# Kernel optimization log

Measured on AMD Instinct MI355X. Metric: run time of the kernel, lower is better.

The kernel has to match this reference:

```python
import jax, jax.numpy as jnp
import numpy as np

# Mamba config (HF defaults for hidden_size=256)
VOCAB = 4096
H = 256          # hidden_size
I = 512          # intermediate_size = 2*H
N = 16           # state_size
R = 16           # time_step_rank = ceil(H/16)
K = 4            # conv_kernel
NUM_LAYERS = 4
B, L = 4, 1024
EPS = 1e-5


def _rmsnorm(x, w):
    return x * jax.lax.rsqrt(jnp.mean(x * x, axis=-1, keepdims=True) + EPS) * w


def setup_inputs() -> dict:
    key = jax.random.key(0)
    ks = jax.random.split(key, 20)
    s = 0.02
    Lyr = NUM_LAYERS
    inp = {
        'input_ids': jax.random.randint(ks[0], (B, L), 0, VOCAB),
        'lengths': jax.random.randint(ks[1], (B,), 1, L + 1),
        'embed': jax.random.normal(ks[2], (VOCAB, H)) * s,
        'norm_w': jnp.ones((Lyr, H)),
        'in_proj_w': jax.random.normal(ks[3], (Lyr, 2 * I, H)) * s,
        'conv_w': jax.random.normal(ks[4], (Lyr, I, K)) * s,
        'conv_b': jnp.zeros((Lyr, I)),
        'x_proj_w': jax.random.normal(ks[5], (Lyr, R + 2 * N, I)) * s,
        'dt_proj_w': jax.random.normal(ks[6], (Lyr, I, R)) * s,
        'dt_proj_b': jax.random.normal(ks[7], (Lyr, I)) * 0.5 - 4.0,
        'A_log': jnp.log(jnp.broadcast_to(jnp.arange(1, N + 1, dtype=jnp.float32), (Lyr, I, N))),
        'D': jnp.ones((Lyr, I)),
        'out_proj_w': jax.random.normal(ks[8], (Lyr, H, I)) * s,
        'final_norm_w': jnp.ones((H,)),
        'head_w1': jax.random.normal(ks[9], (H // 4, H)) * s,
        'head_b1': jnp.zeros((H // 4,)),
        'head_w2': jax.random.normal(ks[10], (1, H // 4)) * s,
        'head_b2': jnp.zeros((1,)),
    }
    return inp


def _mixer(x, in_proj_w, conv_w, conv_b, x_proj_w, dt_proj_w, dt_proj_b, A_log, D_, out_proj_w):
    b, l, _ = x.shape
    proj = x @ in_proj_w.T                      # (b,l,2I)
    xs, gate = proj[..., :I], proj[..., I:]
    # depthwise causal conv1d (kernel K, left pad K-1)
    xp = jnp.pad(xs, ((0, 0), (K - 1, 0), (0, 0)))
    conv = sum(xp[:, k:k + l, :] * conv_w[:, k] for k in range(K))
    xs = jax.nn.silu(conv + conv_b)             # (b,l,I)
    ssm = xs @ x_proj_w.T                       # (b,l,R+2N)
    dt_r, Bmat, Cmat = ssm[..., :R], ssm[..., R:R + N], ssm[..., R + N:]
    dt = jax.nn.softplus(dt_r @ dt_proj_w.T + dt_proj_b)   # (b,l,I)
    A = -jnp.exp(A_log)                         # (I,N)
    dA = jnp.exp(dt[..., None] * A)             # (b,l,I,N)
    dBu = (dt * xs)[..., None] * Bmat[:, :, None, :]        # (b,l,I,N)

    def step(state, inputs):
        a_t, bu_t, c_t = inputs                 # (b,I,N),(b,I,N),(b,N)
        state = a_t * state + bu_t
        y = jnp.einsum('bdn,bn->bd', state, c_t)
        return state, y

    state0 = jnp.zeros((b, I, N), dtype=x.dtype)
    _, ys = jax.lax.scan(step, state0, (dA.transpose(1, 0, 2, 3),
                                        dBu.transpose(1, 0, 2, 3),
                                        Cmat.transpose(1, 0, 2)))
    ys = ys.transpose(1, 0, 2)                  # (b,l,I)
    y = (ys + xs * D_) * jax.nn.silu(gate)
    return y @ out_proj_w.T                     # (b,l,H)


def reference(input_ids, lengths, embed, norm_w, in_proj_w, conv_w, conv_b,
              x_proj_w, dt_proj_w, dt_proj_b, A_log, D, out_proj_w,
              final_norm_w, head_w1, head_b1, head_w2, head_b2):
    h = embed[input_ids]                        # (B,L,H)
    for i in range(NUM_LAYERS):
        res = h
        x = _rmsnorm(h, norm_w[i])
        h = res + _mixer(x, in_proj_w[i], conv_w[i], conv_b[i], x_proj_w[i],
                         dt_proj_w[i], dt_proj_b[i], A_log[i], D[i], out_proj_w[i])
    h = _rmsnorm(h, final_norm_w)
    pooled = h[jnp.arange(h.shape[0]), lengths - 1]         # (B,H)
    hd = jax.nn.gelu(pooled @ head_w1.T + head_b1, approximate=False)
    out = hd @ head_w2.T + head_b2
    return out.squeeze(-1)                      # (B,)
```

## Files before the change

### kernel.cpp

```cpp
#include <hip/hip_runtime.h>
#include <hip/hip_bf16.h>

#define HDIM 256
#define IDIM 512
#define NST 16
#define KCONV 4
#define LAYERS 4
#define BATCH 4
#define LSEQ 1024
#define TOK (BATCH * LSEQ)

typedef unsigned short u16;
typedef float f32x4 __attribute__((ext_vector_type(4)));
typedef short bf16x8 __attribute__((ext_vector_type(8)));

static __device__ __forceinline__ u16 f2bf(float f) {
    __hip_bfloat16 h = __float2bfloat16(f);
    return reinterpret_cast<u16&>(h);
}
static __device__ __forceinline__ float bf2f(u16 b) {
    return __builtin_bit_cast(float, (unsigned)b << 16);
}
static __device__ __forceinline__ float bfup(uint2 u, int j) {
    unsigned w = (j < 2) ? u.x : u.y;
    unsigned bits = (j & 1) ? (w & 0xffff0000u) : (w << 16);
    return __builtin_bit_cast(float, bits);
}

#define DPP_ROW_ADD(p, CTRL)                                                   \
    p += __builtin_bit_cast(float, __builtin_amdgcn_update_dpp(                \
             0, __builtin_bit_cast(int, p), CTRL, 0xf, 0xf, false))

__global__ __launch_bounds__(256) void embed_kernel(const int* __restrict__ ids,
                                                    const float* __restrict__ embed,
                                                    float* __restrict__ h) {
    int idx = blockIdx.x * 256 + threadIdx.x;
    if (idx < TOK * HDIM) {
        int tok = idx >> 8;
        int c = idx & (HDIM - 1);
        h[idx] = embed[ids[tok] * HDIM + c];
    }
}

__global__ __launch_bounds__(256) void cvt4_bf16_kernel(const float* __restrict__ s0, u16* __restrict__ d0,
                                                        const float* __restrict__ s1, u16* __restrict__ d1,
                                                        const float* __restrict__ s2, u16* __restrict__ d2,
                                                        const float* __restrict__ s3, u16* __restrict__ d3) {
    const float* in;
    u16* out;
    int base;
    int bid = blockIdx.x;
    if (bid < 1024)      { in = s0; out = d0; base = bid; }
    else if (bid < 1536) { in = s1; out = d1; base = bid - 1024; }
    else if (bid < 1632) { in = s2; out = d2; base = bid - 1536; }
    else                 { in = s3; out = d3; base = bid - 1632; }
    int j = (base * 256 + threadIdx.x) * 4;
    float4 v = *(const float4*)&in[j];
    unsigned lo = (unsigned)f2bf(v.x) | ((unsigned)f2bf(v.y) << 16);
    unsigned hi = (unsigned)f2bf(v.z) | ((unsigned)f2bf(v.w) << 16);
    *(uint2*)&out[j] = make_uint2(lo, hi);
}

__global__ __launch_bounds__(256) void rmsnorm_kernel(const float* __restrict__ h,
                                                      const float* __restrict__ w,
                                                      u16* __restrict__ xb) {
    int wid = threadIdx.x >> 6, lane = threadIdx.x & 63;
    int tok = blockIdx.x * 4 + wid;
    float4 v = *(const float4*)&h[(size_t)tok * HDIM + lane * 4];
    float s = v.x * v.x + v.y * v.y + v.z * v.z + v.w * v.w;
    #pragma unroll
    for (int m = 32; m >= 1; m >>= 1) s += __shfl_xor(s, m, 64);
    float rstd = rsqrtf(s * (1.0f / HDIM) + 1e-5f);
    float4 wv = *(const float4*)&w[lane * 4];
    unsigned lo = (unsigned)f2bf(v.x * rstd * wv.x) | ((unsigned)f2bf(v.y * rstd * wv.y) << 16);
    unsigned hi = (unsigned)f2bf(v.z * rstd * wv.z) | ((unsigned)f2bf(v.w * rstd * wv.w) << 16);
    *(uint2*)&xb[(size_t)tok * HDIM + lane * 4] = make_uint2(lo, hi);
}

__global__ __launch_bounds__(256) void gemm_bf16_kernel(const u16* __restrict__ A,
                                                        const u16* __restrict__ W,
                                                        u16* __restrict__ C,
                                                        int M, int N, int K) {
    const int BM = 128, BK = 32;
    __shared__ __align__(16) u16 Al[BM][BK + 8];
    __shared__ __align__(16) u16 Bl[BM][BK + 8];
    int m0 = blockIdx.y * BM, n0 = blockIdx.x * BM;
    int tid = threadIdx.x;
    int lane = tid & 63;
    int wid = tid >> 6;
    int wr = wid >> 1, wc = wid & 1;
    int r = lane & 15, g = lane >> 4;

    f32x4 acc[4][4] = {};

    int srow = tid & 127;
    const u16* src = (tid < 128) ? (A + (size_t)(m0 + srow) * K)
                                 : (W + (size_t)(n0 + srow) * K);
    u16* dstrow = (tid < 128) ? &Al[srow][0] : &Bl[srow][0];

    for (int k0 = 0; k0 < K; k0 += BK) {
        uint4 v0 = *(const uint4*)(src + k0);
        uint4 v1 = *(const uint4*)(src + k0 + 8);
        uint4 v2 = *(const uint4*)(src + k0 + 16);
        uint4 v3 = *(const uint4*)(src + k0 + 24);
        __syncthreads();
        *(uint4*)(dstrow)      = v0;
        *(uint4*)(dstrow + 8)  = v1;
        *(uint4*)(dstrow + 16) = v2;
        *(uint4*)(dstrow + 24) = v3;
        __syncthreads();

        bf16x8 af[4], bfr[4];
        #pragma unroll
        for (int f = 0; f < 4; ++f) {
            af[f]  = *(const bf16x8*)&Al[wr * 64 + f * 16 + r][g * 8];
            bfr[f] = *(const bf16x8*)&Bl[wc * 64 + f * 16 + r][g * 8];
        }
        #pragma unroll
        for (int fm = 0; fm < 4; ++fm)
            #pragma unroll
            for (int fn = 0; fn < 4; ++fn)
                acc[fm][fn] = __builtin_amdgcn_mfma_f32_16x16x32_bf16(
                    af[fm], bfr[fn], acc[fm][fn], 0, 0, 0);
    }

    #pragma unroll
    for (int fm = 0; fm < 4; ++fm) {
        #pragma unroll
        for (int fn = 0; fn < 4; ++fn) {
            int col = n0 + wc * 64 + fn * 16 + r;
            #pragma unroll
            for (int v = 0; v < 4; ++v) {
                int row = m0 + wr * 64 + fm * 16 + g * 4 + v;
                C[(size_t)row * N + col] = f2bf(acc[fm][fn][v]);
            }
        }
    }
}

__global__ __launch_bounds__(256) void outproj_norm_kernel(const u16* __restrict__ Y,
                                                           const u16* __restrict__ W,
                                                           const float* __restrict__ nw,
                                                           float* __restrict__ h,
                                                           u16* __restrict__ xb) {
    __shared__ float sH[16][260];
    int m0 = blockIdx.x * 16;
    int tid = threadIdx.x;
    int lane = tid & 63;
    int w = tid >> 6;
    int r = lane & 15, g = lane >> 4;

    f32x4 acc[4] = {};
    const u16* yrow  = Y + (size_t)(m0 + r) * 512 + g * 8;
    const u16* wbase = W + (size_t)(w * 64 + r) * 512 + g * 8;
    #pragma unroll
    for (int k0 = 0; k0 < 512; k0 += 32) {
        bf16x8 af = *(const bf16x8*)(yrow + k0);
        #pragma unroll
        for (int fn = 0; fn < 4; ++fn) {
            bf16x8 bfr = *(const bf16x8*)(wbase + (size_t)fn * 16 * 512 + k0);
            acc[fn] = __builtin_amdgcn_mfma_f32_16x16x32_bf16(af, bfr, acc[fn], 0, 0, 0);
        }
    }

    #pragma unroll
    for (int fn = 0; fn < 4; ++fn) {
        int col = w * 64 + fn * 16 + r;
        #pragma unroll
        for (int v = 0; v < 4; ++v) {
            int row = g * 4 + v;
            size_t off = (size_t)(m0 + row) * HDIM + col;
            float hv = h[off] + acc[fn][v];
            h[off] = hv;
            sH[row][col] = hv;
        }
    }
    __syncthreads();

    int row = tid >> 4, part = tid & 15;
    const float* sr = &sH[row][part * 16];
    float s = 0.f;
    #pragma unroll
    for (int j = 0; j < 16; ++j) s = fmaf(sr[j], sr[j], s);
    DPP_ROW_ADD(s, 0xB1);
    DPP_ROW_ADD(s, 0x4E);
    DPP_ROW_ADD(s, 0x141);
    DPP_ROW_ADD(s, 0x140);
    float rstd = rsqrtf(s * (1.0f / HDIM) + 1e-5f);
    const float* nwp = &nw[part * 16];
    unsigned pk[8];
    #pragma unroll
    for (int j = 0; j < 8; ++j) {
        u16 lo = f2bf(sr[2 * j]     * rstd * nwp[2 * j]);
        u16 hi = f2bf(sr[2 * j + 1] * rstd * nwp[2 * j + 1]);
        pk[j] = (unsigned)lo | ((unsigned)hi << 16);
    }
    u16* dst = xb + (size_t)(m0 + row) * HDIM + part * 16;
    *(uint4*)(dst)     = make_uint4(pk[0], pk[1], pk[2], pk[3]);
    *(uint4*)(dst + 8) = make_uint4(pk[4], pk[5], pk[6], pk[7]);
}

__global__ __launch_bounds__(512) void xproj_kernel(const u16* __restrict__ proj,
                                                    const float* __restrict__ cw,
                                                    const float* __restrict__ cb,
                                                    const u16* __restrict__ W,
                                                    const u16* __restrict__ dtw,
                                                    const float* __restrict__ dtb,
                                                    float* __restrict__ bc,
                                                    float* __restrict__ dtT,
                                                    u16* __restrict__ xs_T,
                                                    u16* __restrict__ gate_T) {
    __shared__ __align__(16) u16 xsL[16][520];
    __shared__ float sP[8][16][52];
    __shared__ float sT[16][52];
    int m0 = blockIdx.x * 16;
    int tid = threadIdx.x;
    int lane = tid & 63;
    int w = tid >> 6;
    int r = lane & 15, g = lane >> 4;
    int tl = m0 & (LSEQ - 1);

    {
        int ic = tid;
        const u16* pxs = proj + (size_t)m0 * 1024 + ic;
        float4 wq = *(const float4*)&cw[ic * 4];
        float bias = cb[ic];
        float a0 = (tl >= 3) ? bf2f(pxs[-3 * 1024]) : 0.f;
        float a1 = (tl >= 2) ? bf2f(pxs[-2 * 1024]) : 0.f;
        float a2 = (tl >= 1) ? bf2f(pxs[-1 * 1024]) : 0.f;
        unsigned xr[8], gr[8];
        #pragma unroll
        for (int t = 0; t < 16; ++t) {
            float a3 = bf2f(pxs[t * 1024]);
            float acc = bias;
            acc = fmaf(a0, wq.x, acc);
            acc = fmaf(a1, wq.y, acc);
            acc = fmaf(a2, wq.z, acc);
            acc = fmaf(a3, wq.w, acc);
            float xsv = acc / (1.f + __expf(-acc));
            u16 xb16 = f2bf(xsv);
            xsL[t][ic] = xb16;
            float gv = bf2f(pxs[t * 1024 + 512]);
            gv = gv / (1.f + __expf(-gv));
            u16 gb16 = f2bf(gv);
            if (t & 1) { xr[t >> 1] |= (unsigned)xb16 << 16; gr[t >> 1] |= (unsigned)gb16 << 16; }
            else       { xr[t >> 1] = xb16;                   gr[t >> 1] = gb16; }
            a0 = a1; a1 = a2; a2 = a3;
        }
        size_t trow = (size_t)ic * TOK + m0;
        *(uint4*)&xs_T[trow]       = make_uint4(xr[0], xr[1], xr[2], xr[3]);
        *(uint4*)&xs_T[trow + 8]   = make_uint4(xr[4], xr[5], xr[6], xr[7]);
        *(uint4*)&gate_T[trow]     = make_uint4(gr[0], gr[1], gr[2], gr[3]);
        *(uint4*)&gate_T[trow + 8] = make_uint4(gr[4], gr[5], gr[6], gr[7]);
    }
    __syncthreads();

    {
        f32x4 acc[3] = {};
        const u16* wbase = W + (size_t)r * 512 + w * 64 + g * 8;
        #pragma unroll
        for (int ks = 0; ks < 2; ++ks) {
            bf16x8 af = *(const bf16x8*)&xsL[r][w * 64 + ks * 32 + g * 8];
            #pragma unroll
            for (int fn = 0; fn < 3; ++fn) {
                bf16x8 bfr = *(const bf16x8*)(wbase + (size_t)fn * 16 * 512 + ks * 32);
                acc[fn] = __builtin_amdgcn_mfma_f32_16x16x32_bf16(af, bfr, acc[fn], 0, 0, 0);
            }
        }
        #pragma unroll
        for (int fn = 0; fn < 3; ++fn)
            #pragma unroll
            for (int v = 0; v < 4; ++v)
                sP[w][g * 4 + v][fn * 16 + r] = acc[fn][v];
    }
    __syncthreads();

    #pragma unroll
    for (int e = 0; e < 2; ++e) {
        int o = tid + e * 512;
        if (o < 768) {
            int row = o / 48, col = o - row * 48;
            float s = 0.f;
            #pragma unroll
            for (int p = 0; p < 8; ++p) s += sP[p][row][col];
            sT[row][col] = s;
        }
    }
    __syncthreads();

    {
        int l = tid;
        int group = l >> 7;
        int rem = l & 127;
        int side = rem >> 6;
        int nn = (rem >> 2) & 15;
        int tq = rem & 3;
        bc[(size_t)blockIdx.x * 512 + l] = sT[group * 4 + tq][16 + side * 16 + nn];
    }

    bf16x8 bv = {};
    if (g < 2) {
        #pragma unroll
        for (int j = 0; j < 8; ++j)
            bv[j] = (short)f2bf(sT[r][g * 8 + j]);
    }
    int mbase = w * 64;
    #pragma unroll
    for (int mf = 0; mf < 4; ++mf) {
        int mrow = mbase + mf * 16;
        bf16x8 av = {};
        if (g < 2) av = *(const bf16x8*)(dtw + (size_t)(mrow + r) * 16 + g * 8);
        f32x4 a2 = __builtin_amdgcn_mfma_f32_16x16x32_bf16(av, bv, f32x4{}, 0, 0, 0);
        float4 b4 = *(const float4*)&dtb[mrow + g * 4];
        #pragma unroll
        for (int v = 0; v < 4; ++v) {
            int i = mrow + g * 4 + v;
            float val = a2[v] + (&b4.x)[v];
            val = fmaxf(val, 0.f) + log1pf(__expf(-fabsf(val)));
            dtT[(size_t)i * TOK + m0 + r] = val;
        }
    }
}

__global__ __launch_bounds__(512) void scan_kernel(const float* __restrict__ dt_T,
                                                   const u16* __restrict__ xs_T,
                                                   const u16* __restrict__ gate_T,
                                                   const float* __restrict__ bc,
                                                   const float* __restrict__ A_log,
                                                   const float* __restrict__ Dw,
                                                   u16* __restrict__ yb) {
    const int NC = 32;
    int n = threadIdx.x & 15;
    int c = threadIdx.x >> 4;

    int lin = (blockIdx.x & 7) * 256 + (blockIdx.x >> 3);
    int b = lin >> 9;
    int i = lin & (IDIM - 1);

    float A = -__expf(A_log[i * NST + n]);

    __shared__ float aprodS[NC][17];
    __shared__ float stendS[NC][17];
    __shared__ float incS[NC][17];

    int t0 = c * 32;
    size_t coff = (size_t)i * TOK + b * LSEQ + t0;
    const float4* dtp = (const float4*)(dt_T + coff);
    const uint2*  xsp = (const uint2*)(xs_T + coff);
    const u16*    xg  = xs_T + coff;
    const u16*    gg  = gate_T + coff;
    const float4* bp  = (const float4*)(bc + (size_t)(b * LSEQ + t0) * 32);

    float dA_r[32], st0_r[32];
    float aprod = 1.f, st = 0.f;
    #pragma unroll
    for (int q = 0; q < 8; ++q) {
        float4 d4 = dtp[q];
        uint2  xu = xsp[q];
        float4 B4 = __builtin_bit_cast(float4, bp[q * 32 + n]);
        #pragma unroll
        for (int j = 0; j < 4; ++j) {
            float dtv = (&d4.x)[j];
            float dA  = __expf(dtv * A);
            dA_r[q * 4 + j] = dA;
            aprod *= dA;
            st = fmaf(dA, st, dtv * bfup(xu, j) * (&B4.x)[j]);
            st0_r[q * 4 + j] = st;
        }
    }
    aprodS[c][n] = aprod;
    stendS[c][n] = st;
    __syncthreads();

    if (threadIdx.x < 16) {
        int nn = threadIdx.x;
        float carry = 0.f;
        for (int cc = 0; cc < NC; ++cc) {
            incS[cc][nn] = carry;
            carry = fmaf(aprodS[cc][nn], carry, stendS[cc][nn]);
        }
    }
    __syncthreads();

    float inc = incS[c][n];
    float cumA = 1.f;
    float Dv = Dw[i];
    u16* y_b = yb + ((size_t)b * LSEQ + t0) * IDIM + i;
    float yacc = 0.f;

    #pragma unroll
    for (int q = 0; q < 8; ++q) {
        float4 C4 = __builtin_bit_cast(float4, bp[q * 32 + 16 + n]);
        #pragma unroll
        for (int j = 0; j < 4; ++j) {
            cumA *= dA_r[q * 4 + j];
            float stv = fmaf(cumA, inc, st0_r[q * 4 + j]);
            float py = stv * (&C4.x)[j];
            DPP_ROW_ADD(py, 0xB1);
            DPP_ROW_ADD(py, 0x4E);
            DPP_ROW_ADD(py, 0x141);
            DPP_ROW_ADD(py, 0x140);
            yacc = (((q & 3) * 4 + j) == n) ? py : yacc;
        }
        if ((q & 3) == 3) {
            int base = (q - 3) * 4;
            float xvn = bf2f(xg[base + n]);
            float gvn = bf2f(gg[base + n]);
            float yv = fmaf(xvn, Dv, yacc) * gvn;
            y_b[(size_t)(base + n) * IDIM] = f2bf(yv);
        }
    }
}

__global__ __launch_bounds__(256) void head_kernel(const float* __restrict__ h,
                                                   const int* __restrict__ lengths,
                                                   const float* __restrict__ fw,
                                                   const float* __restrict__ w1,
                                                   const float* __restrict__ b1,
                                                   const float* __restrict__ w2,
                                                   const float* __restrict__ b2,
                                                   float* __restrict__ out) {
    int b = blockIdx.x;
    int c = threadIdx.x;
    int len = lengths[b];
    const float* row = h + ((size_t)b * LSEQ + (len - 1)) * HDIM;
    float v = row[c];
    float s = v * v;
    #pragma unroll
    for (int m = 32; m >= 1; m >>= 1) s += __shfl_xor(s, m, 64);
    __shared__ float ls[4];
    __shared__ float pooled[HDIM];
    __shared__ float hd[64];
    if ((c & 63) == 0) ls[c >> 6] = s;
    __syncthreads();
    float tot = ls[0] + ls[1] + ls[2] + ls[3];
    float rstd = rsqrtf(tot * (1.0f / HDIM) + 1e-5f);
    pooled[c] = v * rstd * fw[c];
    __syncthreads();
    if (c < 64) {
        float a = b1[c];
        for (int k = 0; k < HDIM; ++k) a = fmaf(pooled[k], w1[c * HDIM + k], a);
        float g = 0.5f * a * (1.f + erff(a * 0.70710678118654752f));
        hd[c] = g * w2[c];
    }
    __syncthreads();
    if (c == 0) {
        float o = b2[0];
        for (int k = 0; k < 64; ++k) o += hd[k];
        out[b] = o;
    }
}

extern "C" void kernel_launch(void* const* d_in, const int* in_sizes, int n_in,
                              void* d_out, int out_size, void* d_ws, size_t ws_size,
                              hipStream_t stream) {
    const int*   ids         = (const int*)d_in[0];
    const int*   lengths     = (const int*)d_in[1];
    const float* embed       = (const float*)d_in[2];
    const float* norm_w      = (const float*)d_in[3];
    const float* in_proj_w   = (const float*)d_in[4];
    const float* conv_w      = (const float*)d_in[5];
    const float* conv_b      = (const float*)d_in[6];
    const float* x_proj_w    = (const float*)d_in[7];
    const float* dt_proj_w   = (const float*)d_in[8];
    const float* dt_proj_b   = (const float*)d_in[9];
    const float* A_log       = (const float*)d_in[10];
    const float* Dw          = (const float*)d_in[11];
    const float* out_proj_w  = (const float*)d_in[12];
    const float* final_norm_w= (const float*)d_in[13];
    const float* head_w1     = (const float*)d_in[14];
    const float* head_b1     = (const float*)d_in[15];
    const float* head_w2     = (const float*)d_in[16];
    const float* head_b2     = (const float*)d_in[17];

    float* ws   = (float*)d_ws;
    float* h    = ws;
    float* dtT  = h    + 1048576;
    float* bc   = dtT  + 2097152;
    u16* xb   = (u16*)(bc + 131072);
    u16* yb   = xb   + 1048576;
    u16* wib  = yb   + 2097152;
    u16* wob  = wib  + 1048576;
    u16* xwb  = wob  + 524288;
    u16* dtwb = xwb  + 98304;
    u16* projb= dtwb + 32768;
    u16* xsT  = projb+ 4194304;
    u16* gT   = xsT  + 2097152;

    embed_kernel<<<TOK * HDIM / 256, 256, 0, stream>>>(ids, embed, h);
    cvt4_bf16_kernel<<<1664, 256, 0, stream>>>(in_proj_w, wib, out_proj_w, wob,
                                               x_proj_w, xwb, dt_proj_w, dtwb);
    rmsnorm_kernel<<<TOK / 4, 256, 0, stream>>>(h, norm_w, xb);

    for (int l = 0; l < LAYERS; ++l) {
        gemm_bf16_kernel<<<dim3(1024 / 128, TOK / 128), 256, 0, stream>>>(
            xb, wib + (size_t)l * 2 * IDIM * HDIM, projb, TOK, 2 * IDIM, HDIM);
        xproj_kernel<<<TOK / 16, 512, 0, stream>>>(
            projb, conv_w + l * IDIM * KCONV, conv_b + l * IDIM,
            xwb + (size_t)l * 48 * IDIM, dtwb + (size_t)l * IDIM * 16,
            dt_proj_b + l * IDIM, bc, dtT, xsT, gT);
        scan_kernel<<<BATCH * IDIM, 512, 0, stream>>>(
            dtT, xsT, gT, bc, A_log + (size_t)l * IDIM * NST, Dw + l * IDIM, yb);
        const float* nw_next = (l + 1 < LAYERS) ? (norm_w + (l + 1) * HDIM) : final_norm_w;
        outproj_norm_kernel<<<TOK / 16, 256, 0, stream>>>(
            yb, wob + (size_t)l * HDIM * IDIM, nw_next, h, xb);
    }

    head_kernel<<<BATCH, 256, 0, stream>>>(h, lengths, final_norm_w,
                                           head_w1, head_b1, head_w2, head_b2,
                                           (float*)d_out);
}
```

Measured before the change: 288.7 us.

## Store scan input xs in fp32 and widen outproj kernel to 8 waves

```diff
diff --git a/kernel.cpp b/kernel.cpp
--- a/kernel.cpp
+++ b/kernel.cpp
@@ -138,7 +138,7 @@
     }
 }
 
-__global__ __launch_bounds__(256) void outproj_norm_kernel(const u16* __restrict__ Y,
+__global__ __launch_bounds__(512) void outproj_norm_kernel(const u16* __restrict__ Y,
                                                            const u16* __restrict__ W,
                                                            const float* __restrict__ nw,
                                                            float* __restrict__ h,
@@ -150,22 +150,22 @@
     int w = tid >> 6;
     int r = lane & 15, g = lane >> 4;
 
-    f32x4 acc[4] = {};
+    f32x4 acc[2] = {};
     const u16* yrow  = Y + (size_t)(m0 + r) * 512 + g * 8;
-    const u16* wbase = W + (size_t)(w * 64 + r) * 512 + g * 8;
+    const u16* wbase = W + (size_t)(w * 32 + r) * 512 + g * 8;
     #pragma unroll
     for (int k0 = 0; k0 < 512; k0 += 32) {
         bf16x8 af = *(const bf16x8*)(yrow + k0);
         #pragma unroll
-        for (int fn = 0; fn < 4; ++fn) {
+        for (int fn = 0; fn < 2; ++fn) {
             bf16x8 bfr = *(const bf16x8*)(wbase + (size_t)fn * 16 * 512 + k0);
             acc[fn] = __builtin_amdgcn_mfma_f32_16x16x32_bf16(af, bfr, acc[fn], 0, 0, 0);
         }
     }
 
     #pragma unroll
-    for (int fn = 0; fn < 4; ++fn) {
-        int col = w * 64 + fn * 16 + r;
+    for (int fn = 0; fn < 2; ++fn) {
+        int col = w * 32 + fn * 16 + r;
         #pragma unroll
         for (int v = 0; v < 4; ++v) {
             int row = g * 4 + v;
@@ -177,27 +177,29 @@
     }
     __syncthreads();
 
-    int row = tid >> 4, part = tid & 15;
-    const float* sr = &sH[row][part * 16];
-    float s = 0.f;
-    #pragma unroll
-    for (int j = 0; j < 16; ++j) s = fmaf(sr[j], sr[j], s);
-    DPP_ROW_ADD(s, 0xB1);
-    DPP_ROW_ADD(s, 0x4E);
-    DPP_ROW_ADD(s, 0x141);
-    DPP_ROW_ADD(s, 0x140);
-    float rstd = rsqrtf(s * (1.0f / HDIM) + 1e-5f);
-    const float* nwp = &nw[part * 16];
-    unsigned pk[8];
-    #pragma unroll
-    for (int j = 0; j < 8; ++j) {
-        u16 lo = f2bf(sr[2 * j]     * rstd * nwp[2 * j]);
-        u16 hi = f2bf(sr[2 * j + 1] * rstd * nwp[2 * j + 1]);
-        pk[j] = (unsigned)lo | ((unsigned)hi << 16);
-    }
-    u16* dst = xb + (size_t)(m0 + row) * HDIM + part * 16;
-    *(uint4*)(dst)     = make_uint4(pk[0], pk[1], pk[2], pk[3]);
-    *(uint4*)(dst + 8) = make_uint4(pk[4], pk[5], pk[6], pk[7]);
+    if (tid < 256) {
+        int row = tid >> 4, part = tid & 15;
+        const float* sr = &sH[row][part * 16];
+        float s = 0.f;
+        #pragma unroll
+        for (int j = 0; j < 16; ++j) s = fmaf(sr[j], sr[j], s);
+        DPP_ROW_ADD(s, 0xB1);
+        DPP_ROW_ADD(s, 0x4E);
+        DPP_ROW_ADD(s, 0x141);
+        DPP_ROW_ADD(s, 0x140);
+        float rstd = rsqrtf(s * (1.0f / HDIM) + 1e-5f);
+        const float* nwp = &nw[part * 16];
+        unsigned pk[8];
+        #pragma unroll
+        for (int j = 0; j < 8; ++j) {
+            u16 lo = f2bf(sr[2 * j]     * rstd * nwp[2 * j]);
+            u16 hi = f2bf(sr[2 * j + 1] * rstd * nwp[2 * j + 1]);
+            pk[j] = (unsigned)lo | ((unsigned)hi << 16);
+        }
+        u16* dst = xb + (size_t)(m0 + row) * HDIM + part * 16;
+        *(uint4*)(dst)     = make_uint4(pk[0], pk[1], pk[2], pk[3]);
+        *(uint4*)(dst + 8) = make_uint4(pk[4], pk[5], pk[6], pk[7]);
+    }
 }
 
 __global__ __launch_bounds__(512) void xproj_kernel(const u16* __restrict__ proj,
@@ -208,7 +210,7 @@
                                                     const float* __restrict__ dtb,
                                                     float* __restrict__ bc,
                                                     float* __restrict__ dtT,
-                                                    u16* __restrict__ xs_T,
+                                                    float* __restrict__ xs_T,
                                                     u16* __restrict__ gate_T) {
     __shared__ __align__(16) u16 xsL[16][520];
     __shared__ float sP[8][16][52];
@@ -228,7 +230,8 @@
         float a0 = (tl >= 3) ? bf2f(pxs[-3 * 1024]) : 0.f;
         float a1 = (tl >= 2) ? bf2f(pxs[-2 * 1024]) : 0.f;
         float a2 = (tl >= 1) ? bf2f(pxs[-1 * 1024]) : 0.f;
-        unsigned xr[8], gr[8];
+        float xf[16];
+        unsigned gr[8];
         #pragma unroll
         for (int t = 0; t < 16; ++t) {
             float a3 = bf2f(pxs[t * 1024]);
@@ -238,18 +241,20 @@
             acc = fmaf(a2, wq.z, acc);
             acc = fmaf(a3, wq.w, acc);
             float xsv = acc / (1.f + __expf(-acc));
-            u16 xb16 = f2bf(xsv);
-            xsL[t][ic] = xb16;
+            xsL[t][ic] = f2bf(xsv);
+            xf[t] = xsv;
             float gv = bf2f(pxs[t * 1024 + 512]);
             gv = gv / (1.f + __expf(-gv));
             u16 gb16 = f2bf(gv);
-            if (t & 1) { xr[t >> 1] |= (unsigned)xb16 << 16; gr[t >> 1] |= (unsigned)gb16 << 16; }
-            else       { xr[t >> 1] = xb16;                   gr[t >> 1] = gb16; }
+            if (t & 1) gr[t >> 1] |= (unsigned)gb16 << 16;
+            else       gr[t >> 1] = gb16;
             a0 = a1; a1 = a2; a2 = a3;
         }
         size_t trow = (size_t)ic * TOK + m0;
-        *(uint4*)&xs_T[trow]       = make_uint4(xr[0], xr[1], xr[2], xr[3]);
-        *(uint4*)&xs_T[trow + 8]   = make_uint4(xr[4], xr[5], xr[6], xr[7]);
+        #pragma unroll
+        for (int q = 0; q < 4; ++q)
+            *(float4*)&xs_T[trow + q * 4] = make_float4(xf[q * 4], xf[q * 4 + 1],
+                                                        xf[q * 4 + 2], xf[q * 4 + 3]);
         *(uint4*)&gate_T[trow]     = make_uint4(gr[0], gr[1], gr[2], gr[3]);
         *(uint4*)&gate_T[trow + 8] = make_uint4(gr[4], gr[5], gr[6], gr[7]);
     }
@@ -323,7 +328,7 @@
 }
 
 __global__ __launch_bounds__(512) void scan_kernel(const float* __restrict__ dt_T,
-                                                   const u16* __restrict__ xs_T,
+                                                   const float* __restrict__ xs_T,
                                                    const u16* __restrict__ gate_T,
                                                    const float* __restrict__ bc,
                                                    const float* __restrict__ A_log,
@@ -346,8 +351,8 @@
     int t0 = c * 32;
     size_t coff = (size_t)i * TOK + b * LSEQ + t0;
     const float4* dtp = (const float4*)(dt_T + coff);
-    const uint2*  xsp = (const uint2*)(xs_T + coff);
-    const u16*    xg  = xs_T + coff;
+    const float4* xsp = (const float4*)(xs_T + coff);
+    const float*  xg  = xs_T + coff;
     const u16*    gg  = gate_T + coff;
     const float4* bp  = (const float4*)(bc + (size_t)(b * LSEQ + t0) * 32);
 
@@ -356,7 +361,7 @@
     #pragma unroll
     for (int q = 0; q < 8; ++q) {
         float4 d4 = dtp[q];
-        uint2  xu = xsp[q];
+        float4 X4 = xsp[q];
         float4 B4 = __builtin_bit_cast(float4, bp[q * 32 + n]);
         #pragma unroll
         for (int j = 0; j < 4; ++j) {
@@ -364,7 +369,7 @@
             float dA  = __expf(dtv * A);
             dA_r[q * 4 + j] = dA;
             aprod *= dA;
-            st = fmaf(dA, st, dtv * bfup(xu, j) * (&B4.x)[j]);
+            st = fmaf(dA, st, dtv * (&X4.x)[j] * (&B4.x)[j]);
             st0_r[q * 4 + j] = st;
         }
     }
@@ -404,7 +409,7 @@
         }
         if ((q & 3) == 3) {
             int base = (q - 3) * 4;
-            float xvn = bf2f(xg[base + n]);
+            float xvn = xg[base + n];
             float gvn = bf2f(gg[base + n]);
             float yv = fmaf(xvn, Dv, yacc) * gvn;
             y_b[(size_t)(base + n) * IDIM] = f2bf(yv);
@@ -477,15 +482,15 @@
     float* h    = ws;
     float* dtT  = h    + 1048576;
     float* bc   = dtT  + 2097152;
-    u16* xb   = (u16*)(bc + 131072);
+    float* xsTf = bc   + 131072;
+    u16* xb   = (u16*)(xsTf + 2097152);
     u16* yb   = xb   + 1048576;
     u16* wib  = yb   + 2097152;
     u16* wob  = wib  + 1048576;
     u16* xwb  = wob  + 524288;
     u16* dtwb = xwb  + 98304;
     u16* projb= dtwb + 32768;
-    u16* xsT  = projb+ 4194304;
-    u16* gT   = xsT  + 2097152;
+    u16* gT   = projb+ 4194304;
 
     embed_kernel<<<TOK * HDIM / 256, 256, 0, stream>>>(ids, embed, h);
     cvt4_bf16_kernel<<<1664, 256, 0, stream>>>(in_proj_w, wib, out_proj_w, wob,
@@ -498,11 +503,11 @@
         xproj_kernel<<<TOK / 16, 512, 0, stream>>>(
             projb, conv_w + l * IDIM * KCONV, conv_b + l * IDIM,
             xwb + (size_t)l * 48 * IDIM, dtwb + (size_t)l * IDIM * 16,
-            dt_proj_b + l * IDIM, bc, dtT, xsT, gT);
+            dt_proj_b + l * IDIM, bc, dtT, xsTf, gT);
         scan_kernel<<<BATCH * IDIM, 512, 0, stream>>>(
-            dtT, xsT, gT, bc, A_log + (size_t)l * IDIM * NST, Dw + l * IDIM, yb);
+            dtT, xsTf, gT, bc, A_log + (size_t)l * IDIM * NST, Dw + l * IDIM, yb);
         const float* nw_next = (l + 1 < LAYERS) ? (norm_w + (l + 1) * HDIM) : final_norm_w;
-        outproj_norm_kernel<<<TOK / 16, 256, 0, stream>>>(
+        outproj_norm_kernel<<<TOK / 16, 512, 0, stream>>>(
             yb, wob + (size_t)l * HDIM * IDIM, nw_next, h, xb);
     }
 
```

Measured after the change: 303.7 us. 5.2% more time.
